# Kernel optimization log

Hardware: AMD Instinct MI355X
Metric: run time of the kernel (lower is better)

The kernel has to match this reference:

```python
import jax, jax.numpy as jnp
import numpy as np

N_NODES = 100000
N_EDGES = 3200000
N_GRAPHS = 256
NODE_DIM = 7
HIDDEN = 64
N_LAYERS = 3
EPS = 1e-5


def setup_inputs() -> dict:
    key = jax.random.key(0)
    ks = jax.random.split(key, 16)
    x = jax.random.normal(ks[0], (N_NODES, NODE_DIM), dtype=jnp.float32)
    edge_index = jax.random.randint(ks[1], (2, N_EDGES), 0, N_NODES, dtype=jnp.int64)
    batch = jnp.sort(jax.random.randint(ks[2], (N_NODES,), 0, N_GRAPHS, dtype=jnp.int64))
    s = 0.05
    return {
        "x": x,
        "edge_index": edge_index,
        "batch": batch,
        "Win": jax.random.normal(ks[3], (NODE_DIM, HIDDEN), jnp.float32) * s,
        "bin_": jnp.zeros((HIDDEN,), jnp.float32),
        "convW": jax.random.normal(ks[4], (N_LAYERS, HIDDEN, HIDDEN), jnp.float32) * s,
        "convB": jnp.zeros((N_LAYERS, HIDDEN), jnp.float32),
        "gnW": jnp.ones((N_LAYERS, HIDDEN), jnp.float32),
        "gnB": jnp.zeros((N_LAYERS, HIDDEN), jnp.float32),
        "gnS": jnp.ones((N_LAYERS, HIDDEN), jnp.float32),
        "clsW1": jax.random.normal(ks[5], (HIDDEN, HIDDEN), jnp.float32) * s,
        "clsB1": jnp.zeros((HIDDEN,), jnp.float32),
        "clsW2": jax.random.normal(ks[6], (HIDDEN, 2), jnp.float32) * s,
        "clsB2": jnp.zeros((2,), jnp.float32),
    }


def _gcn_conv(x, src, dst, W, b):
    # PyG GCNConv: add self-loops, symmetric deg^-1/2 normalization
    loop = jnp.arange(N_NODES, dtype=src.dtype)
    s = jnp.concatenate([src, loop])
    d = jnp.concatenate([dst, loop])
    deg = jax.ops.segment_sum(jnp.ones_like(s, dtype=x.dtype), d, num_segments=N_NODES)
    dinv = jnp.where(deg > 0, jax.lax.rsqrt(deg), 0.0)
    norm = dinv[s] * dinv[d]                      # [E+N]
    xw = x @ W                                    # [N, H]
    msg = xw[s] * norm[:, None]                   # [E+N, H]
    return jax.ops.segment_sum(msg, d, num_segments=N_NODES) + b


def _graph_norm(x, batch, weight, bias, mean_scale):
    cnt = jax.ops.segment_sum(jnp.ones((x.shape[0],), x.dtype), batch, num_segments=N_GRAPHS)
    cnt = jnp.maximum(cnt, 1.0)[:, None]          # [G,1]
    mean = jax.ops.segment_sum(x, batch, num_segments=N_GRAPHS) / cnt
    out = x - mean_scale * mean[batch]
    var = jax.ops.segment_sum(out * out, batch, num_segments=N_GRAPHS) / cnt
    inv_std = jax.lax.rsqrt(var + EPS)
    return weight * out * inv_std[batch] + bias


def reference(x, edge_index, batch, Win, bin_, convW, convB, gnW, gnB, gnS,
              clsW1, clsB1, clsW2, clsB2):
    src, dst = edge_index[0], edge_index[1]
    h = x @ Win + bin_                            # [N, H]
    for i in range(N_LAYERS):
        c = _gcn_conv(h, src, dst, convW[i], convB[i])
        c = _graph_norm(c, batch, gnW[i], gnB[i], gnS[i])
        c = jax.nn.relu(c)
        # dropout: identity (eval mode)
        h = h + c
    cnt = jnp.maximum(
        jax.ops.segment_sum(jnp.ones((h.shape[0],), h.dtype), batch, num_segments=N_GRAPHS), 1.0)
    graph_emb = jax.ops.segment_sum(h, batch, num_segments=N_GRAPHS) / cnt[:, None]  # [G, H]
    z = jax.nn.relu(graph_emb @ clsW1 + clsB1)
    return z @ clsW2 + clsB2                      # [G, 2]
```

## Files before the change

### kernel.cpp

```cpp
#include <hip/hip_runtime.h>
#include <hip/hip_fp16.h>

#define N_NODES 100000
#define N_EDGES 3200000
#define N_GRAPHS 256
#define NODE_DIM 7
#define HID 64
#define NLAY 3
#define EPSV 1e-5f

#define NOCT 8
#define OCT_W 12800
#define BIN_CAP 480000
#define SBW 128
#define NSB 782
#define SB_PER_OCT 100
#define CAP2 4608
#define QDIV 25000
#define NKEY (SBW * 4)

static __device__ __forceinline__ void f4add(float4& a, const float4& b) {
    a.x += b.x; a.y += b.y; a.z += b.z; a.w += b.w;
}

static __device__ __forceinline__ float dot2(unsigned a, unsigned b, float c) {
#if __has_builtin(__builtin_amdgcn_fdot2)
    using h2v = __attribute__((ext_vector_type(2))) _Float16;
    return __builtin_amdgcn_fdot2(__builtin_bit_cast(h2v, a), __builtin_bit_cast(h2v, b), c, false);
#else
    __half2 ha = *(__half2*)&a, hb = *(__half2*)&b;
    float2 fa = __half22float2(ha), fb = __half22float2(hb);
    return fmaf(fa.x, fb.x, fmaf(fa.y, fb.y, c));
#endif
}


__global__ __launch_bounds__(256) void k_gcnt(const int* __restrict__ batch, int* __restrict__ gcnt) {
    __shared__ int start[N_GRAPHS + 1];
    int g = threadIdx.x;
    int lo = 0, hi = N_NODES;
    while (lo < hi) { int mid = (lo + hi) >> 1; if (batch[mid] < g) lo = mid + 1; else hi = mid; }
    start[g] = lo;
    if (g == 0) start[N_GRAPHS] = N_NODES;
    __syncthreads();
    gcnt[g] = start[g + 1] - start[g];
}

__global__ __launch_bounds__(256) void k_bin(const int* __restrict__ src, const int* __restrict__ dst,
                                             int* __restrict__ gcur, int2* __restrict__ bins) {
    __shared__ int lcnt[NOCT];
    __shared__ int lbase[NOCT];
    const int t = threadIdx.x;
    const int NC = N_EDGES / 4 / 256;
    for (int chunk = blockIdx.x; chunk < NC; chunk += gridDim.x) {
        if (t < NOCT) lcnt[t] = 0;
        __syncthreads();
        int i4 = chunk * 256 + t;
        int4 d = ((const int4*)dst)[i4];
        int4 s = ((const int4*)src)[i4];
        int o0 = d.x / OCT_W, o1 = d.y / OCT_W, o2 = d.z / OCT_W, o3 = d.w / OCT_W;
        int r0 = atomicAdd(&lcnt[o0], 1);
        int r1 = atomicAdd(&lcnt[o1], 1);
        int r2 = atomicAdd(&lcnt[o2], 1);
        int r3 = atomicAdd(&lcnt[o3], 1);
        __syncthreads();
        if (t < NOCT) lbase[t] = lcnt[t] ? atomicAdd(&gcur[t], lcnt[t]) : 0;
        __syncthreads();
        bins[(size_t)o0 * BIN_CAP + lbase[o0] + r0] = make_int2(d.x, s.x);
        bins[(size_t)o1 * BIN_CAP + lbase[o1] + r1] = make_int2(d.y, s.y);
        bins[(size_t)o2 * BIN_CAP + lbase[o2] + r2] = make_int2(d.z, s.z);
        bins[(size_t)o3 * BIN_CAP + lbase[o3] + r3] = make_int2(d.w, s.w);
        __syncthreads();
    }
}

__global__ __launch_bounds__(256) void k_bin2a(const int2* __restrict__ bins1, const int* __restrict__ gcur,
                                               int* __restrict__ gcur2, unsigned* __restrict__ bins2) {
    __shared__ int lcnt[SB_PER_OCT];
    __shared__ int lbase[SB_PER_OCT];
    const int o = blockIdx.x & 7;
    const int slice = blockIdx.x >> 3;
    const int t = threadIdx.x;
    const int n = gcur[o];
    const int2* bp = bins1 + (size_t)o * BIN_CAP;
    const int sbBase = o * SB_PER_OCT;
    for (int start = slice * 2048; start < n; start += 32 * 2048) {
        if (t < SB_PER_OCT) lcnt[t] = 0;
        __syncthreads();
        int r[8]; int sbl[8]; unsigned pk[8];
#pragma unroll
        for (int j = 0; j < 8; j++) {
            int idx = start + j * 256 + t;
            if (idx < n) {
                int2 e = bp[idx];
                sbl[j] = (e.x - o * OCT_W) >> 7;
                pk[j] = (unsigned)e.y | ((unsigned)(e.x & (SBW - 1)) << 17);
                r[j] = atomicAdd(&lcnt[sbl[j]], 1);
            } else sbl[j] = -1;
        }
        __syncthreads();
        if (t < SB_PER_OCT) lbase[t] = lcnt[t] ? atomicAdd(&gcur2[sbBase + t], lcnt[t]) : 0;
        __syncthreads();
#pragma unroll
        for (int j = 0; j < 8; j++)
            if (sbl[j] >= 0)
                bins2[(size_t)(sbBase + sbl[j]) * CAP2 + lbase[sbl[j]] + r[j]] = pk[j];
        __syncthreads();
    }
}

__global__ __launch_bounds__(256) void k_bin2s(unsigned* __restrict__ bins2, const int* __restrict__ gcur2,
                                               int* __restrict__ degE, float* __restrict__ dinv,
                                               int* __restrict__ rowptr2) {
    __shared__ unsigned raw[CAP2];
    __shared__ unsigned srt[CAP2];
    __shared__ int cnt[NKEY];
    __shared__ int cur[NKEY];
    const int sb = blockIdx.x;
    const int t = threadIdx.x;
    const int base = sb * SBW;
    int n = gcur2[sb]; if (n > CAP2) n = CAP2;
    unsigned* seg = bins2 + (size_t)sb * CAP2;
    for (int i = t; i < n; i += 256) raw[i] = seg[i];
    for (int i = t; i < NKEY; i += 256) cnt[i] = 0;
    __syncthreads();
    for (int i = t; i < n; i += 256) {
        unsigned p = raw[i];
        int key = (int)(p >> 17) * 4 + (int)((p & 0x1FFFFu) / QDIV);
        atomicAdd(&cnt[key], 1);
    }
    __syncthreads();
    if (t == 0) {
        int run = 0;
        for (int i = 0; i < NKEY; i++) { cur[i] = run; run += cnt[i]; }
    }
    __syncthreads();
    if (t < SBW && base + t < N_NODES) {
        int deg = cnt[t * 4] + cnt[t * 4 + 1] + cnt[t * 4 + 2] + cnt[t * 4 + 3];
        degE[base + t]    = deg;
        dinv[base + t]    = rsqrtf((float)(deg + 1));
        rowptr2[base + t] = sb * CAP2 + cur[t * 4];
    }
    __syncthreads();
    for (int i = t; i < n; i += 256) {
        unsigned p = raw[i];
        int key = (int)(p >> 17) * 4 + (int)((p & 0x1FFFFu) / QDIV);
        srt[atomicAdd(&cur[key], 1)] = p;
    }
    __syncthreads();
    for (int i = t; i < n; i += 256) seg[i] = srt[i];
}


__global__ __launch_bounds__(256) void k_h0(const float* __restrict__ x, const float* __restrict__ Win,
                                            const float* __restrict__ b, float* __restrict__ h) {
    int i = blockIdx.x * 256 + threadIdx.x;
    if (i >= N_NODES * HID) return;
    int v = i >> 6, j = i & 63;
    float acc = b[j];
#pragma unroll
    for (int k = 0; k < NODE_DIM; k++) acc += x[v * NODE_DIM + k] * Win[k * HID + j];
    h[i] = acc;
}

__global__ __launch_bounds__(256) void k_xw(const float* __restrict__ h, const float* __restrict__ W,
                                            const float* __restrict__ dinv, __half* __restrict__ y) {
    __shared__ unsigned Hs2[64][32];
    __shared__ float Ws[HID][HID];
    __shared__ float sdv[64];
    const int t = threadIdx.x;
    const int nb = blockIdx.x * 64;
#pragma unroll
    for (int it = 0; it < 4; it++) {
        int i = t + it * 256;
        ((float4*)Ws)[i] = ((const float4*)W)[i];
        int r = i >> 4, c4 = i & 15;
        int node = nb + r;
        float4 hv = make_float4(0.f, 0.f, 0.f, 0.f);
        if (node < N_NODES) hv = ((const float4*)h)[(size_t)node * 16 + c4];
        __half2 p0 = __floats2half2_rn(hv.x, hv.y);
        __half2 p1 = __floats2half2_rn(hv.z, hv.w);
        Hs2[r][c4 * 2 + 0] = *(unsigned*)&p0;
        Hs2[r][c4 * 2 + 1] = *(unsigned*)&p1;
    }
    if (t < 64) {
        int node = nb + t;
        sdv[t] = (node < N_NODES) ? dinv[node] : 0.f;
    }
    __syncthreads();
    const int j = t & 63;
    const int w = t >> 6;
    unsigned wreg[32];
#pragma unroll
    for (int kp = 0; kp < 32; kp++) {
        __half2 p = __floats2half2_rn(Ws[kp * 2 + 0][j], Ws[kp * 2 + 1][j]);
        wreg[kp] = *(unsigned*)&p;
    }
    for (int nn = 0; nn < 16; nn++) {
        int r = w * 16 + nn;
        int node = nb + r;
        if (node >= N_NODES) break;
        float acc = 0.f;
#pragma unroll
        for (int q = 0; q < 8; q++) {
            uint4 hp = ((const uint4*)&Hs2[r][0])[q];
            acc = dot2(hp.x, wreg[q * 4 + 0], acc);
            acc = dot2(hp.y, wreg[q * 4 + 1], acc);
            acc = dot2(hp.z, wreg[q * 4 + 2], acc);
            acc = dot2(hp.w, wreg[q * 4 + 3], acc);
        }
        y[(size_t)node * HID + j] = __float2half(acc * sdv[r]);
    }
}

__global__ __launch_bounds__(256) void k_agg(const __half* __restrict__ y, const int* __restrict__ rowptr2,
                                             const int* __restrict__ degE, const unsigned* __restrict__ cols,
                                             const float* __restrict__ dinv, const float* __restrict__ bias,
                                             const int* __restrict__ batch, float* __restrict__ c,
                                             float* __restrict__ gS1, float* __restrict__ gS2) {
    __shared__ float sh1[4][HID];
    __shared__ float sh2[4][HID];
    __shared__ int shg[4];
    const int t = threadIdx.x;
    const int w = t >> 6;
    const int lane = t & 63;
    const int v = blockIdx.x * 4 + w;
    const int q = lane >> 3;
    const int f8 = lane & 7;
    const uint4* __restrict__ y16 = (const uint4*)y;

    float a[8] = {0.f,0.f,0.f,0.f,0.f,0.f,0.f,0.f};
    float b[8] = {0.f,0.f,0.f,0.f,0.f,0.f,0.f,0.f};

    auto unpack_add = [&](float* acc, uint4 u) {
        float2 f0 = __half22float2(*(const __half2*)&u.x);
        float2 f1 = __half22float2(*(const __half2*)&u.y);
        float2 f2 = __half22float2(*(const __half2*)&u.z);
        float2 f3 = __half22float2(*(const __half2*)&u.w);
        acc[0] += f0.x; acc[1] += f0.y;
        acc[2] += f1.x; acc[3] += f1.y;
        acc[4] += f2.x; acc[5] += f2.y;
        acc[6] += f3.x; acc[7] += f3.y;
    };

    if (q == 0) unpack_add(a, y16[(size_t)v * 8 + f8]);
    int e0 = rowptr2[v], e1 = e0 + degE[v];
    int e = e0;
    if (e + 31 < e1) {
        int s0 = cols[e + q] & 0x1FFFF, s1 = cols[e + 8 + q] & 0x1FFFF;
        int s2 = cols[e + 16 + q] & 0x1FFFF, s3 = cols[e + 24 + q] & 0x1FFFF;
        for (;;) {
            uint4 u0 = y16[(size_t)s0 * 8 + f8];
            uint4 u1 = y16[(size_t)s1 * 8 + f8];
            uint4 u2 = y16[(size_t)s2 * 8 + f8];
            uint4 u3 = y16[(size_t)s3 * 8 + f8];
            e += 32;
            bool more = (e + 31 < e1);
            if (more) {
                s0 = cols[e + q] & 0x1FFFF; s1 = cols[e + 8 + q] & 0x1FFFF;
                s2 = cols[e + 16 + q] & 0x1FFFF; s3 = cols[e + 24 + q] & 0x1FFFF;
            }
            unpack_add(a, u0);
            unpack_add(b, u1);
            unpack_add(a, u2);
            unpack_add(b, u3);
            if (!more) break;
        }
    }
    if (e + 15 < e1) {
        int s0 = cols[e + q] & 0x1FFFF, s1 = cols[e + 8 + q] & 0x1FFFF;
        uint4 u0 = y16[(size_t)s0 * 8 + f8];
        uint4 u1 = y16[(size_t)s1 * 8 + f8];
        unpack_add(a, u0);
        unpack_add(b, u1);
        e += 16;
    }
    if (e + 7 < e1) {
        unpack_add(a, y16[(size_t)(cols[e + q] & 0x1FFFF) * 8 + f8]);
        e += 8;
    }
    if (e + q < e1) {
        unpack_add(b, y16[(size_t)(cols[e + q] & 0x1FFFF) * 8 + f8]);
    }
#pragma unroll
    for (int k = 0; k < 8; k++) a[k] += b[k];
#pragma unroll
    for (int k = 0; k < 8; k++) {
        a[k] += __shfl_xor(a[k], 8);
        a[k] += __shfl_xor(a[k], 16);
        a[k] += __shfl_xor(a[k], 32);
    }

    if (q == 0) {
        float dv = dinv[v];
        float4 bb0 = ((const float4*)bias)[f8 * 2 + 0];
        float4 bb1 = ((const float4*)bias)[f8 * 2 + 1];
        float cv[8];
        cv[0] = dv * a[0] + bb0.x; cv[1] = dv * a[1] + bb0.y;
        cv[2] = dv * a[2] + bb0.z; cv[3] = dv * a[3] + bb0.w;
        cv[4] = dv * a[4] + bb1.x; cv[5] = dv * a[5] + bb1.y;
        cv[6] = dv * a[6] + bb1.z; cv[7] = dv * a[7] + bb1.w;
        float4* c4 = (float4*)c;
        c4[(size_t)v * 16 + f8 * 2 + 0] = make_float4(cv[0], cv[1], cv[2], cv[3]);
        c4[(size_t)v * 16 + f8 * 2 + 1] = make_float4(cv[4], cv[5], cv[6], cv[7]);
#pragma unroll
        for (int k = 0; k < 8; k++) {
            sh1[w][f8 * 8 + k] = cv[k];
            sh2[w][f8 * 8 + k] = cv[k] * cv[k];
        }
        if (f8 == 0) shg[w] = batch[v];
    }
    __syncthreads();
    if (w == 0) {
        int g0 = shg[0];
        bool uni = (shg[1] == g0) && (shg[2] == g0) && (shg[3] == g0);
        if (uni) {
            float s1 = sh1[0][lane] + sh1[1][lane] + sh1[2][lane] + sh1[3][lane];
            float s2 = sh2[0][lane] + sh2[1][lane] + sh2[2][lane] + sh2[3][lane];
            atomicAdd(&gS1[g0 * HID + lane], s1);
            atomicAdd(&gS2[g0 * HID + lane], s2);
        } else {
#pragma unroll
            for (int ww = 0; ww < 4; ww++) {
                atomicAdd(&gS1[shg[ww] * HID + lane], sh1[ww][lane]);
                atomicAdd(&gS2[shg[ww] * HID + lane], sh2[ww][lane]);
            }
        }
    }
}

__global__ __launch_bounds__(256) void k_stats(const float* __restrict__ gS1, const float* __restrict__ gS2,
                                               const int* __restrict__ gcnt, const float* __restrict__ gnS_l,
                                               float* __restrict__ gmean, float* __restrict__ ginv) {
    int i = blockIdx.x * 256 + threadIdx.x;
    if (i >= N_GRAPHS * HID) return;
    int g = i >> 6, j = i & 63;
    float cnt = fmaxf((float)gcnt[g], 1.f);
    float m = gS1[i] / cnt;
    float s = gnS_l[j];
    float var = gS2[i] / cnt - 2.f * s * m * m + s * s * m * m;
    gmean[i] = m;
    ginv[i] = rsqrtf(var + EPSV);
}

__global__ __launch_bounds__(256) void k_update(const float* __restrict__ c, const int* __restrict__ batch,
                                                const float* __restrict__ gmean, const float* __restrict__ ginv,
                                                const float* __restrict__ gnW_l, const float* __restrict__ gnB_l,
                                                const float* __restrict__ gnS_l, float* __restrict__ h,
                                                float* __restrict__ gemb, int accum_emb) {
    __shared__ float4 shh[16][16];
    __shared__ int shg[16];
    __shared__ int uniS;
    int t = threadIdx.x;
    int i = blockIdx.x * 256 + t;
    int v = i >> 4, f = i & 15, r = t >> 4;
    int g = batch[v];
    float4 c4 = ((const float4*)c)[i];
    float4 m4 = ((const float4*)gmean)[g * 16 + f];
    float4 i4 = ((const float4*)ginv)[g * 16 + f];
    float4 w4 = ((const float4*)gnW_l)[f];
    float4 b4 = ((const float4*)gnB_l)[f];
    float4 s4 = ((const float4*)gnS_l)[f];
    float4 h4 = ((const float4*)h)[i];
    float4 hn;
    hn.x = h4.x + fmaxf(w4.x * (c4.x - s4.x * m4.x) * i4.x + b4.x, 0.f);
    hn.y = h4.y + fmaxf(w4.y * (c4.y - s4.y * m4.y) * i4.y + b4.y, 0.f);
    hn.z = h4.z + fmaxf(w4.z * (c4.z - s4.z * m4.z) * i4.z + b4.z, 0.f);
    hn.w = h4.w + fmaxf(w4.w * (c4.w - s4.w * m4.w) * i4.w + b4.w, 0.f);
    ((float4*)h)[i] = hn;
    if (accum_emb) {
        shh[r][f] = hn;
        if (f == 0) shg[r] = g;
        if (t == 0) uniS = 1;
        __syncthreads();
        if (t < 15 && shg[t + 1] != shg[0]) uniS = 0;
        __syncthreads();
        if (uniS) {
            if (t < 128) f4add(shh[t >> 4][t & 15], shh[(t >> 4) + 8][t & 15]);
            __syncthreads();
            if (t < 64) f4add(shh[t >> 4][t & 15], shh[(t >> 4) + 4][t & 15]);
            __syncthreads();
            if (t < 32) f4add(shh[t >> 4][t & 15], shh[(t >> 4) + 2][t & 15]);
            __syncthreads();
            if (t < 16) {
                f4add(shh[0][t], shh[1][t]);
                float4 s = shh[0][t];
                int g0 = shg[0];
                atomicAdd(&gemb[g0 * HID + t * 4 + 0], s.x);
                atomicAdd(&gemb[g0 * HID + t * 4 + 1], s.y);
                atomicAdd(&gemb[g0 * HID + t * 4 + 2], s.z);
                atomicAdd(&gemb[g0 * HID + t * 4 + 3], s.w);
            }
        } else if (t < 16) {
#pragma unroll
            for (int rr = 0; rr < 16; rr++) {
                float4 s = shh[rr][t];
                int gg = shg[rr];
                atomicAdd(&gemb[gg * HID + t * 4 + 0], s.x);
                atomicAdd(&gemb[gg * HID + t * 4 + 1], s.y);
                atomicAdd(&gemb[gg * HID + t * 4 + 2], s.z);
                atomicAdd(&gemb[gg * HID + t * 4 + 3], s.w);
            }
        }
    }
}

__global__ __launch_bounds__(64) void k_cls(const float* __restrict__ gemb, const int* __restrict__ gcnt,
                                            const float* __restrict__ W1, const float* __restrict__ b1,
                                            const float* __restrict__ W2, const float* __restrict__ b2,
                                            float* __restrict__ out) {
    __shared__ float emb[HID];
    __shared__ float z[HID];
    int g = blockIdx.x, j = threadIdx.x;
    float cnt = fmaxf((float)gcnt[g], 1.f);
    emb[j] = gemb[g * HID + j] / cnt;
    __syncthreads();
    float acc = b1[j];
    for (int k = 0; k < HID; k++) acc += emb[k] * W1[k * HID + j];
    z[j] = fmaxf(acc, 0.f);
    __syncthreads();
    if (j < 2) {
        float o = b2[j];
        for (int k = 0; k < HID; k++) o += z[k] * W2[k * 2 + j];
        out[g * 2 + j] = o;
    }
}

extern "C" void kernel_launch(void* const* d_in, const int* in_sizes, int n_in,
                              void* d_out, int out_size, void* d_ws, size_t ws_size,
                              hipStream_t stream) {
    const float* x     = (const float*)d_in[0];
    const int*   ei    = (const int*)d_in[1];
    const int*   src   = ei;
    const int*   dst   = ei + N_EDGES;
    const int*   batch = (const int*)d_in[2];
    const float* Win   = (const float*)d_in[3];
    const float* bin_  = (const float*)d_in[4];
    const float* convW = (const float*)d_in[5];
    const float* convB = (const float*)d_in[6];
    const float* gnW   = (const float*)d_in[7];
    const float* gnB   = (const float*)d_in[8];
    const float* gnS   = (const float*)d_in[9];
    const float* W1    = (const float*)d_in[10];
    const float* b1    = (const float*)d_in[11];
    const float* W2    = (const float*)d_in[12];
    const float* b2    = (const float*)d_in[13];
    float* out = (float*)d_out;

    char* ws = (char*)d_ws;
    size_t off = 0;
    auto alloc = [&](size_t bytes) -> void* {
        void* p = ws + off;
        off = (off + bytes + 255) & ~(size_t)255;
        return p;
    };
    int*   gcur   = (int*)alloc(NOCT * 4);
    int*   gcur2  = (int*)alloc((size_t)NSB * 4);
    float* gS1    = (float*)alloc((size_t)NLAY * N_GRAPHS * HID * 4);
    float* gS2    = (float*)alloc((size_t)NLAY * N_GRAPHS * HID * 4);
    float* gemb   = (float*)alloc((size_t)N_GRAPHS * HID * 4);
    size_t zeroBytes = off;
    int*   gcnt   = (int*)alloc((size_t)N_GRAPHS * 4);
    int*   degE   = (int*)alloc((size_t)N_NODES * 4);
    float* dinv   = (float*)alloc((size_t)N_NODES * 4);
    int*   rowptr2= (int*)alloc((size_t)N_NODES * 4);
    float* h      = (float*)alloc((size_t)N_NODES * HID * 4);
    __half* y     = (__half*)alloc((size_t)N_NODES * HID * 2);
    float* c      = (float*)alloc((size_t)N_NODES * HID * 4);
    unsigned* bins2 = (unsigned*)alloc((size_t)NSB * CAP2 * 4);
    float* gmean  = (float*)alloc((size_t)N_GRAPHS * HID * 4);
    float* ginv   = (float*)alloc((size_t)N_GRAPHS * HID * 4);
    int2*  bins1  = (int2*)h;
    (void)ws_size; (void)in_sizes; (void)n_in; (void)out_size;

    hipMemsetAsync(d_ws, 0, zeroBytes, stream);

    const int NHB = (N_NODES * HID + 255) / 256;

    k_gcnt<<<1, 256, 0, stream>>>(batch, gcnt);
    k_bin<<<800, 256, 0, stream>>>(src, dst, gcur, bins1);
    k_bin2a<<<256, 256, 0, stream>>>(bins1, gcur, gcur2, bins2);
    k_bin2s<<<NSB, 256, 0, stream>>>(bins2, gcur2, degE, dinv, rowptr2);

    k_h0<<<NHB, 256, 0, stream>>>(x, Win, bin_, h);

    const int XWB = (N_NODES + 63) / 64;
    for (int l = 0; l < NLAY; l++) {
        const float* Wl   = convW + (size_t)l * HID * HID;
        const float* bl   = convB + (size_t)l * HID;
        const float* gnWl = gnW + (size_t)l * HID;
        const float* gnBl = gnB + (size_t)l * HID;
        const float* gnSl = gnS + (size_t)l * HID;
        float* S1l = gS1 + (size_t)l * N_GRAPHS * HID;
        float* S2l = gS2 + (size_t)l * N_GRAPHS * HID;

        k_xw<<<XWB, 256, 0, stream>>>(h, Wl, dinv, y);
        k_agg<<<N_NODES / 4, 256, 0, stream>>>(y, rowptr2, degE, bins2, dinv, bl, batch, c, S1l, S2l);
        k_stats<<<(N_GRAPHS * HID + 255) / 256, 256, 0, stream>>>(S1l, S2l, gcnt, gnSl, gmean, ginv);
        k_update<<<N_NODES * 16 / 256, 256, 0, stream>>>(c, batch, gmean, ginv, gnWl, gnBl, gnSl, h, gemb,
                                                         (l == NLAY - 1) ? 1 : 0);
    }

    k_cls<<<N_GRAPHS, 64, 0, stream>>>(gemb, gcnt, W1, b1, W2, b2, out);
}
```

Measured before the change: 551.7 us.

## Fuse GraphNorm update with next layer's XW and halve aggregation lanes per node

Adds k_upxw, which applies the GraphNorm/ReLU/residual update to h and immediately computes the next layer's fp16 XW product from shared memory, saving one kernel launch and one reread of h per intermediate layer. The aggregation kernel now gives each node half a wavefront (32 lanes, 4 edge groups) instead of a full wavefront, handling 8 nodes per block. Edge indices are read with nontemporal loads. The narrower split means fewer lanes per node for high-degree nodes, and the fused kernel carries more shared memory and register use.

```diff
diff --git a/kernel.cpp b/kernel.cpp
--- a/kernel.cpp
+++ b/kernel.cpp
@@ -213,20 +213,90 @@
     }
 }
 
+__global__ __launch_bounds__(256) void k_upxw(const float* __restrict__ c, const int* __restrict__ batch,
+                                              const float* __restrict__ gmean, const float* __restrict__ ginv,
+                                              const float* __restrict__ gnW_l, const float* __restrict__ gnB_l,
+                                              const float* __restrict__ gnS_l, float* __restrict__ h,
+                                              const float* __restrict__ W, const float* __restrict__ dinv,
+                                              __half* __restrict__ y) {
+    __shared__ unsigned Hs2[64][32];
+    __shared__ float Ws[HID][HID];
+    __shared__ float sdv[64];
+    const int t = threadIdx.x;
+    const int nb = blockIdx.x * 64;
+#pragma unroll
+    for (int it = 0; it < 4; it++) {
+        int i = t + it * 256;
+        ((float4*)Ws)[i] = ((const float4*)W)[i];
+        int r = i >> 4, f = i & 15;
+        int node = nb + r;
+        float4 hn = make_float4(0.f, 0.f, 0.f, 0.f);
+        if (node < N_NODES) {
+            int g = batch[node];
+            float4 h4 = ((const float4*)h)[(size_t)node * 16 + f];
+            float4 cv = ((const float4*)c)[(size_t)node * 16 + f];
+            float4 m4 = ((const float4*)gmean)[g * 16 + f];
+            float4 i4 = ((const float4*)ginv)[g * 16 + f];
+            float4 w4 = ((const float4*)gnW_l)[f];
+            float4 b4 = ((const float4*)gnB_l)[f];
+            float4 s4 = ((const float4*)gnS_l)[f];
+            hn.x = h4.x + fmaxf(w4.x * (cv.x - s4.x * m4.x) * i4.x + b4.x, 0.f);
+            hn.y = h4.y + fmaxf(w4.y * (cv.y - s4.y * m4.y) * i4.y + b4.y, 0.f);
+            hn.z = h4.z + fmaxf(w4.z * (cv.z - s4.z * m4.z) * i4.z + b4.z, 0.f);
+            hn.w = h4.w + fmaxf(w4.w * (cv.w - s4.w * m4.w) * i4.w + b4.w, 0.f);
+            ((float4*)h)[(size_t)node * 16 + f] = hn;
+        }
+        __half2 p0 = __floats2half2_rn(hn.x, hn.y);
+        __half2 p1 = __floats2half2_rn(hn.z, hn.w);
+        Hs2[r][f * 2 + 0] = *(unsigned*)&p0;
+        Hs2[r][f * 2 + 1] = *(unsigned*)&p1;
+    }
+    if (t < 64) {
+        int node = nb + t;
+        sdv[t] = (node < N_NODES) ? dinv[node] : 0.f;
+    }
+    __syncthreads();
+    const int j = t & 63;
+    const int w = t >> 6;
+    unsigned wreg[32];
+#pragma unroll
+    for (int kp = 0; kp < 32; kp++) {
+        __half2 p = __floats2half2_rn(Ws[kp * 2 + 0][j], Ws[kp * 2 + 1][j]);
+        wreg[kp] = *(unsigned*)&p;
+    }
+    for (int nn = 0; nn < 16; nn++) {
+        int r = w * 16 + nn;
+        int node = nb + r;
+        if (node >= N_NODES) break;
+        float acc = 0.f;
+#pragma unroll
+        for (int q = 0; q < 8; q++) {
+            uint4 hp = ((const uint4*)&Hs2[r][0])[q];
+            acc = dot2(hp.x, wreg[q * 4 + 0], acc);
+            acc = dot2(hp.y, wreg[q * 4 + 1], acc);
+            acc = dot2(hp.z, wreg[q * 4 + 2], acc);
+            acc = dot2(hp.w, wreg[q * 4 + 3], acc);
+        }
+        y[(size_t)node * HID + j] = __float2half(acc * sdv[r]);
+    }
+}
+
 __global__ __launch_bounds__(256) void k_agg(const __half* __restrict__ y, const int* __restrict__ rowptr2,
                                              const int* __restrict__ degE, const unsigned* __restrict__ cols,
                                              const float* __restrict__ dinv, const float* __restrict__ bias,
                                              const int* __restrict__ batch, float* __restrict__ c,
                                              float* __restrict__ gS1, float* __restrict__ gS2) {
-    __shared__ float sh1[4][HID];
-    __shared__ float sh2[4][HID];
-    __shared__ int shg[4];
+    __shared__ float sh1[8][HID];
+    __shared__ float sh2[8][HID];
+    __shared__ int shg[8];
     const int t = threadIdx.x;
     const int w = t >> 6;
     const int lane = t & 63;
-    const int v = blockIdx.x * 4 + w;
-    const int q = lane >> 3;
-    const int f8 = lane & 7;
+    const int half = lane >> 5;
+    const int hl = lane & 31;
+    const int v = blockIdx.x * 8 + w * 2 + half;
+    const int g4 = hl >> 3;
+    const int f8 = hl & 7;
     const uint4* __restrict__ y16 = (const uint4*)y;
 
     float a[8] = {0.f,0.f,0.f,0.f,0.f,0.f,0.f,0.f};
@@ -243,44 +313,36 @@
         acc[6] += f3.x; acc[7] += f3.y;
     };
 
-    if (q == 0) unpack_add(a, y16[(size_t)v * 8 + f8]);
-    int e0 = rowptr2[v], e1 = e0 + degE[v];
-    int e = e0;
-    if (e + 31 < e1) {
-        int s0 = cols[e + q] & 0x1FFFF, s1 = cols[e + 8 + q] & 0x1FFFF;
-        int s2 = cols[e + 16 + q] & 0x1FFFF, s3 = cols[e + 24 + q] & 0x1FFFF;
-        for (;;) {
-            uint4 u0 = y16[(size_t)s0 * 8 + f8];
-            uint4 u1 = y16[(size_t)s1 * 8 + f8];
-            uint4 u2 = y16[(size_t)s2 * 8 + f8];
-            uint4 u3 = y16[(size_t)s3 * 8 + f8];
-            e += 32;
-            bool more = (e + 31 < e1);
-            if (more) {
-                s0 = cols[e + q] & 0x1FFFF; s1 = cols[e + 8 + q] & 0x1FFFF;
-                s2 = cols[e + 16 + q] & 0x1FFFF; s3 = cols[e + 24 + q] & 0x1FFFF;
-            }
-            unpack_add(a, u0);
-            unpack_add(b, u1);
-            unpack_add(a, u2);
-            unpack_add(b, u3);
-            if (!more) break;
-        }
-    }
-    if (e + 15 < e1) {
-        int s0 = cols[e + q] & 0x1FFFF, s1 = cols[e + 8 + q] & 0x1FFFF;
+    if (g4 == 0) unpack_add(a, y16[(size_t)v * 8 + f8]);
+    const int e0 = rowptr2[v], e1 = e0 + degE[v];
+    int e = e0 + g4;
+    while (e + 12 < e1) {
+        int s0 = (int)(__builtin_nontemporal_load(cols + e)      & 0x1FFFFu);
+        int s1 = (int)(__builtin_nontemporal_load(cols + e + 4)  & 0x1FFFFu);
+        int s2 = (int)(__builtin_nontemporal_load(cols + e + 8)  & 0x1FFFFu);
+        int s3 = (int)(__builtin_nontemporal_load(cols + e + 12) & 0x1FFFFu);
+        uint4 u0 = y16[(size_t)s0 * 8 + f8];
+        uint4 u1 = y16[(size_t)s1 * 8 + f8];
+        uint4 u2 = y16[(size_t)s2 * 8 + f8];
+        uint4 u3 = y16[(size_t)s3 * 8 + f8];
+        unpack_add(a, u0);
+        unpack_add(b, u1);
+        unpack_add(a, u2);
+        unpack_add(b, u3);
+        e += 16;
+    }
+    while (e + 4 < e1) {
+        int s0 = (int)(__builtin_nontemporal_load(cols + e)     & 0x1FFFFu);
+        int s1 = (int)(__builtin_nontemporal_load(cols + e + 4) & 0x1FFFFu);
         uint4 u0 = y16[(size_t)s0 * 8 + f8];
         uint4 u1 = y16[(size_t)s1 * 8 + f8];
         unpack_add(a, u0);
         unpack_add(b, u1);
-        e += 16;
-    }
-    if (e + 7 < e1) {
-        unpack_add(a, y16[(size_t)(cols[e + q] & 0x1FFFF) * 8 + f8]);
         e += 8;
     }
-    if (e + q < e1) {
-        unpack_add(b, y16[(size_t)(cols[e + q] & 0x1FFFF) * 8 + f8]);
+    if (e < e1) {
+        int s0 = (int)(__builtin_nontemporal_load(cols + e) & 0x1FFFFu);
+        unpack_add(a, y16[(size_t)s0 * 8 + f8]);
     }
 #pragma unroll
     for (int k = 0; k < 8; k++) a[k] += b[k];
@@ -288,10 +350,10 @@
     for (int k = 0; k < 8; k++) {
         a[k] += __shfl_xor(a[k], 8);
         a[k] += __shfl_xor(a[k], 16);
-        a[k] += __shfl_xor(a[k], 32);
-    }
-
-    if (q == 0) {
+    }
+
+    const int row = w * 2 + half;
+    if (g4 == 0) {
         float dv = dinv[v];
         float4 bb0 = ((const float4*)bias)[f8 * 2 + 0];
         float4 bb1 = ((const float4*)bias)[f8 * 2 + 1];
@@ -305,23 +367,26 @@
         c4[(size_t)v * 16 + f8 * 2 + 1] = make_float4(cv[4], cv[5], cv[6], cv[7]);
 #pragma unroll
         for (int k = 0; k < 8; k++) {
-            sh1[w][f8 * 8 + k] = cv[k];
-            sh2[w][f8 * 8 + k] = cv[k] * cv[k];
-        }
-        if (f8 == 0) shg[w] = batch[v];
+            sh1[row][f8 * 8 + k] = cv[k];
+            sh2[row][f8 * 8 + k] = cv[k] * cv[k];
+        }
+        if (f8 == 0) shg[row] = batch[v];
     }
     __syncthreads();
     if (w == 0) {
         int g0 = shg[0];
-        bool uni = (shg[1] == g0) && (shg[2] == g0) && (shg[3] == g0);
+        bool uni = true;
+#pragma unroll
+        for (int ww = 1; ww < 8; ww++) uni = uni && (shg[ww] == g0);
         if (uni) {
-            float s1 = sh1[0][lane] + sh1[1][lane] + sh1[2][lane] + sh1[3][lane];
-            float s2 = sh2[0][lane] + sh2[1][lane] + sh2[2][lane] + sh2[3][lane];
+            float s1 = 0.f, s2 = 0.f;
+#pragma unroll
+            for (int ww = 0; ww < 8; ww++) { s1 += sh1[ww][lane]; s2 += sh2[ww][lane]; }
             atomicAdd(&gS1[g0 * HID + lane], s1);
             atomicAdd(&gS2[g0 * HID + lane], s2);
         } else {
 #pragma unroll
-            for (int ww = 0; ww < 4; ww++) {
+            for (int ww = 0; ww < 8; ww++) {
                 atomicAdd(&gS1[shg[ww] * HID + lane], sh1[ww][lane]);
                 atomicAdd(&gS2[shg[ww] * HID + lane], sh2[ww][lane]);
             }
@@ -347,7 +412,7 @@
                                                 const float* __restrict__ gmean, const float* __restrict__ ginv,
                                                 const float* __restrict__ gnW_l, const float* __restrict__ gnB_l,
                                                 const float* __restrict__ gnS_l, float* __restrict__ h,
-                                                float* __restrict__ gemb, int accum_emb) {
+                                                float* __restrict__ gemb) {
     __shared__ float4 shh[16][16];
     __shared__ int shg[16];
     __shared__ int uniS;
@@ -368,39 +433,37 @@
     hn.z = h4.z + fmaxf(w4.z * (c4.z - s4.z * m4.z) * i4.z + b4.z, 0.f);
     hn.w = h4.w + fmaxf(w4.w * (c4.w - s4.w * m4.w) * i4.w + b4.w, 0.f);
     ((float4*)h)[i] = hn;
-    if (accum_emb) {
-        shh[r][f] = hn;
-        if (f == 0) shg[r] = g;
-        if (t == 0) uniS = 1;
-        __syncthreads();
-        if (t < 15 && shg[t + 1] != shg[0]) uniS = 0;
-        __syncthreads();
-        if (uniS) {
-            if (t < 128) f4add(shh[t >> 4][t & 15], shh[(t >> 4) + 8][t & 15]);
-            __syncthreads();
-            if (t < 64) f4add(shh[t >> 4][t & 15], shh[(t >> 4) + 4][t & 15]);
-            __syncthreads();
-            if (t < 32) f4add(shh[t >> 4][t & 15], shh[(t >> 4) + 2][t & 15]);
-            __syncthreads();
-            if (t < 16) {
-                f4add(shh[0][t], shh[1][t]);
-                float4 s = shh[0][t];
-                int g0 = shg[0];
-                atomicAdd(&gemb[g0 * HID + t * 4 + 0], s.x);
-                atomicAdd(&gemb[g0 * HID + t * 4 + 1], s.y);
-                atomicAdd(&gemb[g0 * HID + t * 4 + 2], s.z);
-                atomicAdd(&gemb[g0 * HID + t * 4 + 3], s.w);
-            }
-        } else if (t < 16) {
-#pragma unroll
-            for (int rr = 0; rr < 16; rr++) {
-                float4 s = shh[rr][t];
-                int gg = shg[rr];
-                atomicAdd(&gemb[gg * HID + t * 4 + 0], s.x);
-                atomicAdd(&gemb[gg * HID + t * 4 + 1], s.y);
-                atomicAdd(&gemb[gg * HID + t * 4 + 2], s.z);
-                atomicAdd(&gemb[gg * HID + t * 4 + 3], s.w);
-            }
+    shh[r][f] = hn;
+    if (f == 0) shg[r] = g;
+    if (t == 0) uniS = 1;
+    __syncthreads();
+    if (t < 15 && shg[t + 1] != shg[0]) uniS = 0;
+    __syncthreads();
+    if (uniS) {
+        if (t < 128) f4add(shh[t >> 4][t & 15], shh[(t >> 4) + 8][t & 15]);
+        __syncthreads();
+        if (t < 64) f4add(shh[t >> 4][t & 15], shh[(t >> 4) + 4][t & 15]);
+        __syncthreads();
+        if (t < 32) f4add(shh[t >> 4][t & 15], shh[(t >> 4) + 2][t & 15]);
+        __syncthreads();
+        if (t < 16) {
+            f4add(shh[0][t], shh[1][t]);
+            float4 s = shh[0][t];
+            int g0 = shg[0];
+            atomicAdd(&gemb[g0 * HID + t * 4 + 0], s.x);
+            atomicAdd(&gemb[g0 * HID + t * 4 + 1], s.y);
+            atomicAdd(&gemb[g0 * HID + t * 4 + 2], s.z);
+            atomicAdd(&gemb[g0 * HID + t * 4 + 3], s.w);
+        }
+    } else if (t < 16) {
+#pragma unroll
+        for (int rr = 0; rr < 16; rr++) {
+            float4 s = shh[rr][t];
+            int gg = shg[rr];
+            atomicAdd(&gemb[gg * HID + t * 4 + 0], s.x);
+            atomicAdd(&gemb[gg * HID + t * 4 + 1], s.y);
+            atomicAdd(&gemb[gg * HID + t * 4 + 2], s.z);
+            atomicAdd(&gemb[gg * HID + t * 4 + 3], s.w);
         }
     }
 }
@@ -485,8 +548,8 @@
     k_h0<<<NHB, 256, 0, stream>>>(x, Win, bin_, h);
 
     const int XWB = (N_NODES + 63) / 64;
+    k_xw<<<XWB, 256, 0, stream>>>(h, convW, dinv, y);
     for (int l = 0; l < NLAY; l++) {
-        const float* Wl   = convW + (size_t)l * HID * HID;
         const float* bl   = convB + (size_t)l * HID;
         const float* gnWl = gnW + (size_t)l * HID;
         const float* gnBl = gnB + (size_t)l * HID;
@@ -494,11 +557,15 @@
         float* S1l = gS1 + (size_t)l * N_GRAPHS * HID;
         float* S2l = gS2 + (size_t)l * N_GRAPHS * HID;
 
-        k_xw<<<XWB, 256, 0, stream>>>(h, Wl, dinv, y);
-        k_agg<<<N_NODES / 4, 256, 0, stream>>>(y, rowptr2, degE, bins2, dinv, bl, batch, c, S1l, S2l);
+        k_agg<<<N_NODES / 8, 256, 0, stream>>>(y, rowptr2, degE, bins2, dinv, bl, batch, c, S1l, S2l);
         k_stats<<<(N_GRAPHS * HID + 255) / 256, 256, 0, stream>>>(S1l, S2l, gcnt, gnSl, gmean, ginv);
-        k_update<<<N_NODES * 16 / 256, 256, 0, stream>>>(c, batch, gmean, ginv, gnWl, gnBl, gnSl, h, gemb,
-                                                         (l == NLAY - 1) ? 1 : 0);
+        if (l < NLAY - 1) {
+            const float* Wn = convW + (size_t)(l + 1) * HID * HID;
+            k_upxw<<<XWB, 256, 0, stream>>>(c, batch, gmean, ginv, gnWl, gnBl, gnSl, h, Wn, dinv, y);
+        } else {
+            k_update<<<N_NODES * 16 / 256, 256, 0, stream>>>(c, batch, gmean, ginv, gnWl, gnBl, gnSl,
+                                                             h, gemb);
+        }
     }
 
     k_cls<<<N_GRAPHS, 64, 0, stream>>>(gemb, gcnt, W1, b1, W2, b2, out);
```

New measurement: 498.6 us. 9.6% less time.
